# Optimization experiments

Hardware: AMD Instinct MI355X
Metric: run time of the kernel (lower is better)

Reference implementation:

```python
import jax, jax.numpy as jnp
import numpy as np

B, N, D, H, M, CD = 2, 2048, 1024, 16, 77, 768
DH = D // H          # head dim 64
FF = 4 * D           # GEGLU hidden 4096
NBITS = 8
EPS = 1e-5


def fake_quant_w(w, n_bits=NBITS):
    """Per-tensor uniform affine INT8 fake-quant (UniformAffineQuantizerINT8) with STE."""
    levels = 2 ** n_bits - 1
    mn = jnp.min(w)
    mx = jnp.max(w)
    delta = (mx - mn) / levels
    zp = jnp.round(-mn / delta)
    wq = jnp.clip(jnp.round(w / delta) + zp, 0, levels)
    wdq = (wq - zp) * delta
    return w + jax.lax.stop_gradient(wdq - w)


def layernorm(x, g, b):
    mu = jnp.mean(x, axis=-1, keepdims=True)
    var = jnp.mean((x - mu) ** 2, axis=-1, keepdims=True)
    return (x - mu) * jax.lax.rsqrt(var + EPS) * g + b


def linear(x, w, b=None):
    y = x @ fake_quant_w(w).T
    return y if b is None else y + b


def cross_attn(x, ctx, qw, kw, vw, ow, ob):
    Bq, Nq, _ = x.shape
    Nk = ctx.shape[1]
    q = linear(x, qw).reshape(Bq, Nq, H, DH)     # b n h d
    k = linear(ctx, kw).reshape(Bq, Nk, H, DH)
    v = linear(ctx, vw).reshape(Bq, Nk, H, DH)
    scale = DH ** -0.5
    sim = jnp.einsum('bihd,bjhd->bhij', q, k) * scale   # [B,H,Nq,Nk]
    attn = jax.nn.softmax(sim, axis=-1)
    out = jnp.einsum('bhij,bjhd->bihd', attn, v).reshape(Bq, Nq, D)
    return linear(out, ow, ob)


def geglu_ff(x, w1, b1, w2, b2):
    h = linear(x, w1, b1)                # [B,N,2*FF]
    hidden, gate = jnp.split(h, 2, axis=-1)
    return linear(hidden * jax.nn.gelu(gate), w2, b2)


def setup_inputs() -> dict:
    key = jax.random.key(0)
    ks = jax.random.split(key, 24)
    W = lambda k, o, i: (jax.random.normal(k, (o, i), jnp.float32) * 0.02)
    return {
        'x': jax.random.normal(ks[0], (B, N, D), jnp.float32),
        'context': jax.random.normal(ks[1], (B, M, CD), jnp.float32),
        'ln1_g': 1.0 + 0.1 * jax.random.normal(ks[2], (D,), jnp.float32),
        'ln1_b': 0.1 * jax.random.normal(ks[3], (D,), jnp.float32),
        'ln2_g': 1.0 + 0.1 * jax.random.normal(ks[4], (D,), jnp.float32),
        'ln2_b': 0.1 * jax.random.normal(ks[5], (D,), jnp.float32),
        'ln3_g': 1.0 + 0.1 * jax.random.normal(ks[6], (D,), jnp.float32),
        'ln3_b': 0.1 * jax.random.normal(ks[7], (D,), jnp.float32),
        'q1_w': W(ks[8], D, D), 'k1_w': W(ks[9], D, D), 'v1_w': W(ks[10], D, D),
        'o1_w': W(ks[11], D, D), 'o1_b': jnp.zeros((D,), jnp.float32),
        'q2_w': W(ks[12], D, D), 'k2_w': W(ks[13], D, CD), 'v2_w': W(ks[14], D, CD),
        'o2_w': W(ks[15], D, D), 'o2_b': jnp.zeros((D,), jnp.float32),
        'ff1_w': W(ks[16], 2 * FF, D), 'ff1_b': jnp.zeros((2 * FF,), jnp.float32),
        'ff2_w': W(ks[17], D, FF), 'ff2_b': jnp.zeros((D,), jnp.float32),
    }


def reference(x, context, ln1_g, ln1_b, ln2_g, ln2_b, ln3_g, ln3_b,
              q1_w, k1_w, v1_w, o1_w, o1_b,
              q2_w, k2_w, v2_w, o2_w, o2_b,
              ff1_w, ff1_b, ff2_w, ff2_b):
    x = cross_attn(layernorm(x, ln1_g, ln1_b), layernorm(x, ln1_g, ln1_b),
                   q1_w, k1_w, v1_w, o1_w, o1_b) + x
    x = cross_attn(layernorm(x, ln2_g, ln2_b), context,
                   q2_w, k2_w, v2_w, o2_w, o2_b) + x
    x = geglu_ff(layernorm(x, ln3_g, ln3_b), ff1_w, ff1_b, ff2_w, ff2_b) + x
    return x
```

## Files before the change

kernel.cpp:

```cpp
#include <hip/hip_runtime.h>
#include <cstdint>
#include <cstddef>

typedef unsigned short ushort_t;
typedef short s16x8 __attribute__((ext_vector_type(8)));
typedef float f32x4 __attribute__((ext_vector_type(4)));
typedef unsigned u32x4 __attribute__((ext_vector_type(4)));

#define MFMA(A,B,C) __builtin_amdgcn_mfma_f32_16x16x32_bf16((A),(B),(C),0,0,0)

__device__ __forceinline__ float b2f(ushort_t h){ return __uint_as_float(((unsigned)h)<<16); }
__device__ __forceinline__ ushort_t f2b(float f){
  unsigned u = __float_as_uint(f);
  u += 0x7FFFu + ((u >> 16) & 1u);
  return (ushort_t)(u >> 16);
}
__device__ __forceinline__ unsigned f2o(float f){
  unsigned u = __float_as_uint(f);
  return (u & 0x80000000u) ? ~u : (u | 0x80000000u);
}
__device__ __forceinline__ float o2f(unsigned u){
  unsigned b = (u & 0x80000000u) ? (u & 0x7FFFFFFFu) : ~u;
  return __uint_as_float(b);
}

struct QT { const float* w[10]; ushort_t* o[10]; int n[10]; };

__global__ void init_k(unsigned* slots){
  int t = threadIdx.x;
  if (t < 20) slots[t] = (t & 1) ? 0u : 0xFFFFFFFFu;
}

__global__ __launch_bounds__(256) void minmax_k(QT qt, unsigned* slots){
  int t = blockIdx.y;
  const float4* w = (const float4*)qt.w[t];
  int n4 = qt.n[t] >> 2;
  float mn = 3.4e38f, mx = -3.4e38f;
  for (int i = blockIdx.x*256 + threadIdx.x; i < n4; i += gridDim.x*256){
    float4 v = w[i];
    mn = fminf(mn, fminf(fminf(v.x, v.y), fminf(v.z, v.w)));
    mx = fmaxf(mx, fmaxf(fmaxf(v.x, v.y), fmaxf(v.z, v.w)));
  }
  #pragma unroll
  for (int o = 1; o < 64; o <<= 1){
    mn = fminf(mn, __shfl_xor(mn, o));
    mx = fmaxf(mx, __shfl_xor(mx, o));
  }
  __shared__ float smn[4], smx[4];
  int wv = threadIdx.x >> 6;
  if ((threadIdx.x & 63) == 0){ smn[wv] = mn; smx[wv] = mx; }
  __syncthreads();
  if (threadIdx.x == 0){
    mn = fminf(fminf(smn[0], smn[1]), fminf(smn[2], smn[3]));
    mx = fmaxf(fmaxf(smx[0], smx[1]), fmaxf(smx[2], smx[3]));
    atomicMin(&slots[2*t], f2o(mn));
    atomicMax(&slots[2*t+1], f2o(mx));
  }
}

__global__ __launch_bounds__(256) void dequant_k(QT qt, const unsigned* __restrict__ slots){
  int t = blockIdx.y;
  float mn = o2f(slots[2*t]), mx = o2f(slots[2*t+1]);
  float delta = (mx - mn) * (1.f/255.f);
  float zp = rintf(-mn / delta);
  const float4* w = (const float4*)qt.w[t];
  ushort4* o = (ushort4*)qt.o[t];
  int n4 = qt.n[t] >> 2;
  for (int i = blockIdx.x*256 + threadIdx.x; i < n4; i += gridDim.x*256){
    float4 v = w[i];
    ushort4 r;
    float q;
    q = fminf(fmaxf(rintf(v.x/delta) + zp, 0.f), 255.f); r.x = f2b((q - zp)*delta);
    q = fminf(fmaxf(rintf(v.y/delta) + zp, 0.f), 255.f); r.y = f2b((q - zp)*delta);
    q = fminf(fmaxf(rintf(v.z/delta) + zp, 0.f), 255.f); r.z = f2b((q - zp)*delta);
    q = fminf(fmaxf(rintf(v.w/delta) + zp, 0.f), 255.f); r.w = f2b((q - zp)*delta);
    o[i] = r;
  }
}

__global__ __launch_bounds__(256) void f2b_k(const float* __restrict__ in, ushort_t* __restrict__ out, int n4){
  for (int i = blockIdx.x*256 + threadIdx.x; i < n4; i += gridDim.x*256){
    float4 v = ((const float4*)in)[i];
    ushort4 r; r.x = f2b(v.x); r.y = f2b(v.y); r.z = f2b(v.z); r.w = f2b(v.w);
    ((ushort4*)out)[i] = r;
  }
}

__global__ __launch_bounds__(256) void ln_k(const float* __restrict__ x, const float* __restrict__ g,
                                            const float* __restrict__ b, ushort_t* __restrict__ out){
  int row = blockIdx.x, tid = threadIdx.x;
  float4 v = ((const float4*)(x + (size_t)row*1024))[tid];
  float s  = v.x + v.y + v.z + v.w;
  float s2 = v.x*v.x + v.y*v.y + v.z*v.z + v.w*v.w;
  #pragma unroll
  for (int o = 1; o < 64; o <<= 1){ s += __shfl_xor(s, o); s2 += __shfl_xor(s2, o); }
  __shared__ float rs[4], rs2[4];
  int wv = tid >> 6;
  if ((tid & 63) == 0){ rs[wv] = s; rs2[wv] = s2; }
  __syncthreads();
  s = rs[0]+rs[1]+rs[2]+rs[3]; s2 = rs2[0]+rs2[1]+rs2[2]+rs2[3];
  float mu = s * (1.f/1024.f);
  float var = s2 * (1.f/1024.f) - mu*mu;
  float rstd = rsqrtf(var + 1e-5f);
  float4 gv = ((const float4*)g)[tid], bv = ((const float4*)b)[tid];
  ushort4 r;
  r.x = f2b((v.x - mu)*rstd*gv.x + bv.x);
  r.y = f2b((v.y - mu)*rstd*gv.y + bv.y);
  r.z = f2b((v.z - mu)*rstd*gv.z + bv.z);
  r.w = f2b((v.w - mu)*rstd*gv.w + bv.w);
  ((ushort4*)(out + (size_t)row*1024))[tid] = r;
}

__global__ __launch_bounds__(512) void gemm_k(
    const ushort_t* __restrict__ A, const ushort_t* __restrict__ W,
    const float* __restrict__ bias, const float* __restrict__ resid,
    float* __restrict__ outF, ushort_t* __restrict__ outB,
    int M, int N, int K, int lda, int ldw)
{
  __shared__ ushort_t As[3][256*32];
  __shared__ ushort_t Bs[3][128*32];
  const int tid = threadIdx.x;
  const int lane = tid & 63, wv = tid >> 6;
  const int g = lane >> 4, qi = lane & 15;

  const int gx = gridDim.x, gy = gridDim.y;
  const int lid = blockIdx.x + blockIdx.y * gx;
  int m0, n0;
  if (((gx & 3) | (gy & 1)) == 0){
    const int w = gx >> 2, h = gy >> 1;
    const int xcd = lid & 7, o = lid >> 3;
    const int cx = xcd & 3, cy = xcd >> 2;
    n0 = (cx * w + (o % w)) * 128;
    m0 = (cy * h + (o / w)) * 256;
  } else {
    n0 = blockIdx.x * 128;
    m0 = blockIdx.y * 256;
  }

  const int koff = blockIdx.z * K;
  if (gridDim.z > 1) outF += (size_t)blockIdx.z * M * N;

  const int wr = (wv >> 1) * 64, wc = (wv & 1) * 64;
  f32x4 acc[4][4] = {};

  const int ra0 = tid >> 2,        sa0 = (tid & 3) ^ ((ra0 >> 1) & 3);
  const int ra1 = (512+tid) >> 2,  sa1 = ((512+tid) & 3) ^ ((ra1 >> 1) & 3);
  const int aA0 = (m0 + ra0 < M) ? m0 + ra0 : M - 1;
  const int aA1 = (m0 + ra1 < M) ? m0 + ra1 : M - 1;
  const size_t dA0 = (size_t)tid*8, dA1 = (size_t)(512+tid)*8, dB0 = (size_t)tid*8;

  #define GSTAGE(bi_, kt_) do {                                                    \
    __builtin_amdgcn_global_load_lds(                                              \
      (const __attribute__((address_space(1))) void*)(A + (size_t)aA0*lda + koff + (kt_) + sa0*8), \
      (__attribute__((address_space(3))) void*)(&As[bi_][dA0]), 16, 0, 0);         \
    __builtin_amdgcn_global_load_lds(                                              \
      (const __attribute__((address_space(1))) void*)(A + (size_t)aA1*lda + koff + (kt_) + sa1*8), \
      (__attribute__((address_space(3))) void*)(&As[bi_][dA1]), 16, 0, 0);         \
    __builtin_amdgcn_global_load_lds(                                              \
      (const __attribute__((address_space(1))) void*)(W + (size_t)(n0 + ra0)*ldw + koff + (kt_) + sa0*8), \
      (__attribute__((address_space(3))) void*)(&Bs[bi_][dB0]), 16, 0, 0);         \
  } while(0)

  const int nt = K >> 5;
  GSTAGE(0, 0);
  if (nt > 1) GSTAGE(1, 32);
  if (nt > 1) asm volatile("s_waitcnt vmcnt(3)" ::: "memory");
  else        asm volatile("s_waitcnt vmcnt(0)" ::: "memory");
  __builtin_amdgcn_s_barrier();
  __builtin_amdgcn_sched_barrier(0);

  int bi = 0;
  for (int t = 0; t < nt; ++t){
    int b2 = bi + 2; if (b2 >= 3) b2 -= 3;
    if (t + 2 < nt) GSTAGE(b2, (t + 2) << 5);
    s16x8 af[4], bfr[4];
    #pragma unroll
    for (int mi = 0; mi < 4; ++mi){
      int row = wr + mi*16 + qi;
      int sl = g ^ ((row >> 1) & 3);
      af[mi] = *(const s16x8*)(&As[bi][row*32 + sl*8]);
    }
    #pragma unroll
    for (int ni = 0; ni < 4; ++ni){
      int row = wc + ni*16 + qi;
      int sl = g ^ ((row >> 1) & 3);
      bfr[ni] = *(const s16x8*)(&Bs[bi][row*32 + sl*8]);
    }
    __builtin_amdgcn_s_setprio(1);
    #pragma unroll
    for (int mi = 0; mi < 4; ++mi)
      #pragma unroll
      for (int ni = 0; ni < 4; ++ni)
        acc[mi][ni] = MFMA(af[mi], bfr[ni], acc[mi][ni]);
    __builtin_amdgcn_s_setprio(0);
    if (t + 1 < nt){
      if (t + 2 < nt) asm volatile("s_waitcnt vmcnt(3)" ::: "memory");
      else            asm volatile("s_waitcnt vmcnt(0)" ::: "memory");
      __builtin_amdgcn_s_barrier();
      __builtin_amdgcn_sched_barrier(0);
    }
    bi += 1; if (bi >= 3) bi -= 3;
  }
  #undef GSTAGE

  #pragma unroll
  for (int mi = 0; mi < 4; ++mi){
    #pragma unroll
    for (int r = 0; r < 4; ++r){
      int row = m0 + wr + mi*16 + g*4 + r;
      if (row >= M) continue;
      #pragma unroll
      for (int ni = 0; ni < 4; ++ni){
        int col = n0 + wc + ni*16 + qi;
        float v = acc[mi][ni][r];
        if (bias)  v += bias[col];
        if (resid) v += resid[(size_t)row*N + col];
        if (outF)  outF[(size_t)row*N + col] = v;
        else       outB[(size_t)row*N + col] = f2b(v);
      }
    }
  }
}

__global__ __launch_bounds__(256) void reduce_k(const float* __restrict__ p0, const float* __restrict__ p1,
                                                const float* __restrict__ bias, const float* __restrict__ resid,
                                                float* __restrict__ outF, ushort_t* __restrict__ outB, int n4){
  for (int i = blockIdx.x*256 + threadIdx.x; i < n4; i += gridDim.x*256){
    float4 a = ((const float4*)p0)[i];
    float4 b = ((const float4*)p1)[i];
    float4 v;
    v.x = a.x + b.x; v.y = a.y + b.y; v.z = a.z + b.z; v.w = a.w + b.w;
    if (bias){
      float4 bb = ((const float4*)bias)[i & 255];
      v.x += bb.x; v.y += bb.y; v.z += bb.z; v.w += bb.w;
    }
    if (resid){
      float4 r = ((const float4*)resid)[i];
      v.x += r.x; v.y += r.y; v.z += r.z; v.w += r.w;
    }
    if (outF) ((float4*)outF)[i] = v;
    else {
      ushort4 o; o.x = f2b(v.x); o.y = f2b(v.y); o.z = f2b(v.z); o.w = f2b(v.w);
      ((ushort4*)outB)[i] = o;
    }
  }
}

__global__ __launch_bounds__(256) void vtrans_k(const ushort_t* __restrict__ src, ushort_t* __restrict__ dst,
                                                int rows, int stride, int col_off, int nk_pad){
  __shared__ ushort_t ldst[64*130];
  int n0 = blockIdx.x * 128;
  int b = blockIdx.y >> 4, h = blockIdx.y & 15;
  const ushort_t* s = src + (size_t)b*rows*stride + col_off + h*64;
  for (int idx = threadIdx.x; idx < 128*64; idx += 256){
    int n = idx >> 6, d = idx & 63;
    int ng = n0 + n;
    ushort_t v = (ng < rows) ? s[(size_t)ng*stride + d] : (ushort_t)0;
    ldst[d*130 + n] = v;
  }
  __syncthreads();
  ushort_t* o = dst + (size_t)(b*16 + h)*64*nk_pad;
  for (int idx = threadIdx.x; idx < 64*128; idx += 256){
    int d = idx >> 7, n = idx & 127;
    if (n0 + n < nk_pad) o[(size_t)d*nk_pad + n0 + n] = ldst[d*130 + n];
  }
}

__global__ __launch_bounds__(256) void attn_k(
    const ushort_t* __restrict__ Q, const ushort_t* __restrict__ Kp, const ushort_t* __restrict__ Vt,
    ushort_t* __restrict__ O, int nq, int nk, int qstride, int kvstride, int nk_pad)
{
  __shared__ ushort_t Ks[2][32*64];
  __shared__ ushort_t Vs[2][64*32];
  const int tid = threadIdx.x, lane = tid & 63, wv = tid >> 6;
  const int g = lane >> 4, qi = lane & 15;
  const int b = blockIdx.y >> 4, h = blockIdx.y & 15;
  const int q0 = blockIdx.x*64 + wv*16;

  const ushort_t* Qr = Q + (size_t)(b*nq + q0 + qi)*qstride + h*64;
  s16x8 qf0 = *(const s16x8*)(Qr + g*8);
  s16x8 qf1 = *(const s16x8*)(Qr + 32 + g*8);
  const ushort_t* Kb = Kp + (size_t)b*nk*kvstride + h*64;
  const ushort_t* Vb = Vt + (size_t)(b*16 + h)*64*nk_pad;

  const int krow = wv*8 + (lane >> 3);
  const int kgsl = (lane & 7) ^ (krow & 7);
  const int vrow = wv*16 + (lane >> 2);
  const int vgsl = (lane & 3) ^ ((vrow >> 1) & 3);

  #define STAGE(buf, kb_) do {                                                   \
    int kr_ = (kb_) + krow; if (kr_ >= nk) kr_ = nk - 1;                         \
    __builtin_amdgcn_global_load_lds(                                            \
      (const __attribute__((address_space(1))) void*)(Kb + (size_t)kr_*kvstride + kgsl*8), \
      (__attribute__((address_space(3))) void*)(&Ks[buf][(size_t)wv*512]), 16, 0, 0); \
    __builtin_amdgcn_global_load_lds(                                            \
      (const __attribute__((address_space(1))) void*)(Vb + (size_t)vrow*nk_pad + (kb_) + vgsl*8), \
      (__attribute__((address_space(3))) void*)(&Vs[buf][(size_t)wv*512]), 16, 0, 0); \
  } while(0)

  const int nkp = (nk + 31) & ~31;
  f32x4 ot[4] = {};
  float m_run = -1e30f, l_run = 0.f;
  const float SC = 0.18033688011f;

  const int ks0 = (g     ^ (qi & 7)) * 8;
  const int ks1 = ((4+g) ^ (qi & 7)) * 8;
  const int vs0 = (g ^ ((qi >> 1) & 3)) * 8;

  STAGE(0, 0);
  asm volatile("s_waitcnt vmcnt(0)" ::: "memory");
  __syncthreads();
  int cur = 0;
  for (int kb = 0; kb < nkp; kb += 32){
    if (kb + 32 < nkp) STAGE(cur^1, kb + 32);
    s16x8 ka0 = *(const s16x8*)(&Ks[cur][(qi)*64      + ks0]);
    s16x8 ka1 = *(const s16x8*)(&Ks[cur][(qi)*64      + ks1]);
    s16x8 kb0 = *(const s16x8*)(&Ks[cur][(16+qi)*64   + ks0]);
    s16x8 kb1 = *(const s16x8*)(&Ks[cur][(16+qi)*64   + ks1]);
    s16x8 vf0 = *(const s16x8*)(&Vs[cur][(qi)*32      + vs0]);
    s16x8 vf1 = *(const s16x8*)(&Vs[cur][(16+qi)*32   + vs0]);
    s16x8 vf2 = *(const s16x8*)(&Vs[cur][(32+qi)*32   + vs0]);
    s16x8 vf3 = *(const s16x8*)(&Vs[cur][(48+qi)*32   + vs0]);

    f32x4 st0 = {}, st1 = {};
    st0 = MFMA(ka0, qf0, st0);
    st0 = MFMA(ka1, qf1, st0);
    st1 = MFMA(kb0, qf0, st1);
    st1 = MFMA(kb1, qf1, st1);
    float s[8];
    #pragma unroll
    for (int r = 0; r < 4; ++r){ s[r] = st0[r]*SC; s[4+r] = st1[r]*SC; }
    if (kb + 32 > nk){
      #pragma unroll
      for (int r = 0; r < 4; ++r){
        if (kb + 4*g + r >= nk)      s[r]   = -1e30f;
        if (kb + 16 + 4*g + r >= nk) s[4+r] = -1e30f;
      }
    }
    float bm = fmaxf(fmaxf(fmaxf(s[0], s[1]), fmaxf(s[2], s[3])),
                     fmaxf(fmaxf(s[4], s[5]), fmaxf(s[6], s[7])));
    bm = fmaxf(bm, __shfl_xor(bm, 16));
    bm = fmaxf(bm, __shfl_xor(bm, 32));
    if (!__all(bm <= m_run)){
      float m_new = fmaxf(m_run, bm);
      float fac = exp2f(m_run - m_new);
      l_run *= fac;
      #pragma unroll
      for (int dd = 0; dd < 4; ++dd)
        #pragma unroll
        for (int r = 0; r < 4; ++r) ot[dd][r] *= fac;
      m_run = m_new;
    }
    float p[8], rsum = 0.f;
    #pragma unroll
    for (int i = 0; i < 8; ++i){ p[i] = exp2f(s[i] - m_run); rsum += p[i]; }
    rsum += __shfl_xor(rsum, 16);
    rsum += __shfl_xor(rsum, 32);
    l_run += rsum;
    unsigned pk[4];
    #pragma unroll
    for (int r = 0; r < 4; ++r)
      pk[r] = (unsigned)f2b(p[r]) | ((unsigned)f2b(p[4+r]) << 16);
    int srcbase = ((2*g) & 3) * 16 + qi;
    unsigned sh0[4], sh1[4];
    #pragma unroll
    for (int r = 0; r < 4; ++r){
      sh0[r] = (unsigned)__shfl((int)pk[r], srcbase);
      sh1[r] = (unsigned)__shfl((int)pk[r], srcbase + 16);
    }
    unsigned sel = (g >> 1) ? 0x07060302u : 0x05040100u;
    u32x4 pw;
    pw[0] = __builtin_amdgcn_perm(sh0[1], sh0[0], sel);
    pw[1] = __builtin_amdgcn_perm(sh0[3], sh0[2], sel);
    pw[2] = __builtin_amdgcn_perm(sh1[1], sh1[0], sel);
    pw[3] = __builtin_amdgcn_perm(sh1[3], sh1[2], sel);
    s16x8 pf = __builtin_bit_cast(s16x8, pw);
    ot[0] = MFMA(vf0, pf, ot[0]);
    ot[1] = MFMA(vf1, pf, ot[1]);
    ot[2] = MFMA(vf2, pf, ot[2]);
    ot[3] = MFMA(vf3, pf, ot[3]);

    asm volatile("s_waitcnt vmcnt(0)" ::: "memory");
    __syncthreads();
    cur ^= 1;
  }
  #undef STAGE
  float inv = 1.f / l_run;
  ushort_t* Or = O + (size_t)(b*nq + q0 + qi)*1024 + h*64;
  #pragma unroll
  for (int dd = 0; dd < 4; ++dd)
    #pragma unroll
    for (int r = 0; r < 4; ++r)
      Or[dd*16 + 4*g + r] = f2b(ot[dd][r] * inv);
}

__global__ __launch_bounds__(256) void geglu_k(const ushort_t* __restrict__ h, ushort_t* __restrict__ out){
  int idx = blockIdx.x*256 + threadIdx.x;
  int r = idx >> 9, c = idx & 511;
  s16x8 hv = *(const s16x8*)(h + (size_t)r*8192 + c*8);
  s16x8 gv = *(const s16x8*)(h + (size_t)r*8192 + 4096 + c*8);
  s16x8 o;
  #pragma unroll
  for (int i = 0; i < 8; ++i){
    float gg = b2f((ushort_t)gv[i]);
    float t  = 0.7978845608f*(gg + 0.044715f*gg*gg*gg);
    float e  = __expf(2.f*t);
    float th = 1.f - 2.f/(e + 1.f);
    float ge = 0.5f*gg*(1.f + th);
    o[i] = (short)f2b(b2f((ushort_t)hv[i]) * ge);
  }
  *(s16x8*)(out + (size_t)r*4096 + c*8) = o;
}

extern "C" void kernel_launch(void* const* d_in, const int* in_sizes, int n_in,
                              void* d_out, int out_size, void* d_ws, size_t ws_size,
                              hipStream_t stream)
{
  const float* x    = (const float*)d_in[0];
  const float* ctx  = (const float*)d_in[1];
  const float* ln1g = (const float*)d_in[2];
  const float* ln1b = (const float*)d_in[3];
  const float* ln2g = (const float*)d_in[4];
  const float* ln2b = (const float*)d_in[5];
  const float* ln3g = (const float*)d_in[6];
  const float* ln3b = (const float*)d_in[7];
  const float* q1w  = (const float*)d_in[8];
  const float* k1w  = (const float*)d_in[9];
  const float* v1w  = (const float*)d_in[10];
  const float* o1w  = (const float*)d_in[11];
  const float* o1b  = (const float*)d_in[12];
  const float* q2w  = (const float*)d_in[13];
  const float* k2w  = (const float*)d_in[14];
  const float* v2w  = (const float*)d_in[15];
  const float* o2w  = (const float*)d_in[16];
  const float* o2b  = (const float*)d_in[17];
  const float* ff1w = (const float*)d_in[18];
  const float* ff1b = (const float*)d_in[19];
  const float* ff2w = (const float*)d_in[20];
  const float* ff2b = (const float*)d_in[21];

  char* base = (char*)d_ws;
  size_t off = 0;
  auto alloc = [&](size_t bytes) -> char* {
    char* p = base + off;
    off += (bytes + 255) & ~(size_t)255;
    return p;
  };
  unsigned*  slots = (unsigned*)alloc(80);
  ushort_t*  ctxb  = (ushort_t*)alloc((size_t)154*768*2);
  ushort_t*  wqkv1 = (ushort_t*)alloc((size_t)3072*1024*2);
  ushort_t*  o1d   = (ushort_t*)alloc((size_t)1024*1024*2);
  ushort_t*  q2d   = (ushort_t*)alloc((size_t)1024*1024*2);
  ushort_t*  wkv2  = (ushort_t*)alloc((size_t)2048*768*2);
  ushort_t*  o2d   = (ushort_t*)alloc((size_t)1024*1024*2);
  ushort_t*  f1d   = (ushort_t*)alloc((size_t)8192*1024*2);
  ushort_t*  f2d   = (ushort_t*)alloc((size_t)1024*4096*2);
  ushort_t*  lnb   = (ushort_t*)alloc((size_t)4096*1024*2);
  ushort_t*  qkvb  = (ushort_t*)alloc((size_t)4096*3072*2);
  ushort_t*  q2b   = (ushort_t*)alloc((size_t)4096*1024*2);
  ushort_t*  atb   = (ushort_t*)alloc((size_t)4096*1024*2);
  ushort_t*  kvb   = (ushort_t*)alloc((size_t)154*2048*2);
  ushort_t*  vt1   = (ushort_t*)alloc((size_t)2*16*64*2048*2);
  ushort_t*  vt2   = (ushort_t*)alloc((size_t)2*16*64*96*2);
  float*     x1    = (float*)alloc((size_t)4096*1024*4);
  float*     x2    = (float*)alloc((size_t)4096*1024*4);
  ushort_t*  hb    = (ushort_t*)alloc((size_t)4096*8192*2);
  ushort_t*  actb  = qkvb;
  float*     part  = (float*)hb;
  float*     part1 = part + (size_t)4096*1024;

  QT qt;
  qt.w[0]=q1w;  qt.o[0]=wqkv1;               qt.n[0]=1024*1024;
  qt.w[1]=k1w;  qt.o[1]=wqkv1+1024*1024;     qt.n[1]=1024*1024;
  qt.w[2]=v1w;  qt.o[2]=wqkv1+2*1024*1024;   qt.n[2]=1024*1024;
  qt.w[3]=o1w;  qt.o[3]=o1d;                 qt.n[3]=1024*1024;
  qt.w[4]=q2w;  qt.o[4]=q2d;                 qt.n[4]=1024*1024;
  qt.w[5]=k2w;  qt.o[5]=wkv2;                qt.n[5]=1024*768;
  qt.w[6]=v2w;  qt.o[6]=wkv2+1024*768;       qt.n[6]=1024*768;
  qt.w[7]=o2w;  qt.o[7]=o2d;                 qt.n[7]=1024*1024;
  qt.w[8]=ff1w; qt.o[8]=f1d;                 qt.n[8]=8192*1024;
  qt.w[9]=ff2w; qt.o[9]=f2d;                 qt.n[9]=1024*4096;

  init_k<<<1, 64, 0, stream>>>(slots);
  minmax_k<<<dim3(64,10), 256, 0, stream>>>(qt, slots);
  dequant_k<<<dim3(64,10), 256, 0, stream>>>(qt, slots);
  f2b_k<<<64, 256, 0, stream>>>(ctx, ctxb, 154*768/4);

  ln_k<<<4096, 256, 0, stream>>>(x, ln1g, ln1b, lnb);
  gemm_k<<<dim3(24, 16), 512, 0, stream>>>(lnb, wqkv1, nullptr, nullptr,
                                           nullptr, qkvb, 4096, 3072, 1024, 1024, 1024);
  vtrans_k<<<dim3(16, 32), 256, 0, stream>>>(qkvb, vt1, 2048, 3072, 2048, 2048);
  attn_k<<<dim3(32, 32), 256, 0, stream>>>(qkvb, qkvb+1024, vt1, atb,
                                           2048, 2048, 3072, 3072, 2048);
  gemm_k<<<dim3(8, 16, 2), 512, 0, stream>>>(atb, o1d, nullptr, nullptr,
                                             part, nullptr, 4096, 1024, 512, 1024, 1024);
  reduce_k<<<2048, 256, 0, stream>>>(part, part1, o1b, x, x1, nullptr, 4096*1024/4);

  ln_k<<<4096, 256, 0, stream>>>(x1, ln2g, ln2b, lnb);
  gemm_k<<<dim3(8, 16, 2), 512, 0, stream>>>(lnb, q2d, nullptr, nullptr,
                                             part, nullptr, 4096, 1024, 512, 1024, 1024);
  reduce_k<<<2048, 256, 0, stream>>>(part, part1, nullptr, nullptr, nullptr, q2b, 4096*1024/4);
  gemm_k<<<dim3(16, 1), 512, 0, stream>>>(ctxb, wkv2, nullptr, nullptr,
                                          nullptr, kvb, 154, 2048, 768, 768, 768);
  vtrans_k<<<dim3(1, 32), 256, 0, stream>>>(kvb, vt2, 77, 2048, 1024, 96);
  attn_k<<<dim3(32, 32), 256, 0, stream>>>(q2b, kvb, vt2, atb,
                                           2048, 77, 1024, 2048, 96);
  gemm_k<<<dim3(8, 16, 2), 512, 0, stream>>>(atb, o2d, nullptr, nullptr,
                                             part, nullptr, 4096, 1024, 512, 1024, 1024);
  reduce_k<<<2048, 256, 0, stream>>>(part, part1, o2b, x1, x2, nullptr, 4096*1024/4);

  ln_k<<<4096, 256, 0, stream>>>(x2, ln3g, ln3b, lnb);
  gemm_k<<<dim3(64, 16), 512, 0, stream>>>(lnb, f1d, ff1b, nullptr,
                                           nullptr, hb, 4096, 8192, 1024, 1024, 1024);
  geglu_k<<<8192, 256, 0, stream>>>(hb, actb);
  gemm_k<<<dim3(8, 16, 2), 512, 0, stream>>>(actb, f2d, nullptr, nullptr,
                                             part, nullptr, 4096, 1024, 2048, 4096, 4096);
  reduce_k<<<2048, 256, 0, stream>>>(part, part1, ff2b, x2,
                                     (float*)d_out, nullptr, 4096*1024/4);
}
```

Measured before the change: 633.2 us.

## Fold softmax scale into Q weights and enlarge attention blocks to 8 waves

The softmax scale (including log2e) is folded into the dequantized Q projection weights, which removes the per-score multiply inside attention. Attention blocks grow from 4 to 8 waves covering 128 queries, so each K/V tile staged in shared memory serves twice as many queries, and the staging work is split so four waves load K and four load V. exp2f is replaced by the hardware exp2 builtin. Folding the scale before bf16 rounding of the weights changes rounding slightly, and the larger blocks halve the grid, which may reduce occupancy.

```diff
diff --git a/kernel.cpp b/kernel.cpp
--- a/kernel.cpp
+++ b/kernel.cpp
@@ -24,7 +24,7 @@
   return __uint_as_float(b);
 }
 
-struct QT { const float* w[10]; ushort_t* o[10]; int n[10]; };
+struct QT { const float* w[10]; ushort_t* o[10]; int n[10]; float os[10]; };
 
 __global__ void init_k(unsigned* slots){
   int t = threadIdx.x;
@@ -63,6 +63,7 @@
   float mn = o2f(slots[2*t]), mx = o2f(slots[2*t+1]);
   float delta = (mx - mn) * (1.f/255.f);
   float zp = rintf(-mn / delta);
+  float osc = qt.os[t];
   const float4* w = (const float4*)qt.w[t];
   ushort4* o = (ushort4*)qt.o[t];
   int n4 = qt.n[t] >> 2;
@@ -70,10 +71,10 @@
     float4 v = w[i];
     ushort4 r;
     float q;
-    q = fminf(fmaxf(rintf(v.x/delta) + zp, 0.f), 255.f); r.x = f2b((q - zp)*delta);
-    q = fminf(fmaxf(rintf(v.y/delta) + zp, 0.f), 255.f); r.y = f2b((q - zp)*delta);
-    q = fminf(fmaxf(rintf(v.z/delta) + zp, 0.f), 255.f); r.z = f2b((q - zp)*delta);
-    q = fminf(fmaxf(rintf(v.w/delta) + zp, 0.f), 255.f); r.w = f2b((q - zp)*delta);
+    q = fminf(fmaxf(rintf(v.x/delta) + zp, 0.f), 255.f); r.x = f2b((q - zp)*delta*osc);
+    q = fminf(fmaxf(rintf(v.y/delta) + zp, 0.f), 255.f); r.y = f2b((q - zp)*delta*osc);
+    q = fminf(fmaxf(rintf(v.z/delta) + zp, 0.f), 255.f); r.z = f2b((q - zp)*delta*osc);
+    q = fminf(fmaxf(rintf(v.w/delta) + zp, 0.f), 255.f); r.w = f2b((q - zp)*delta*osc);
     o[i] = r;
   }
 }
@@ -266,7 +267,7 @@
   }
 }
 
-__global__ __launch_bounds__(256) void attn_k(
+__global__ __launch_bounds__(512) void attn_k(
     const ushort_t* __restrict__ Q, const ushort_t* __restrict__ Kp, const ushort_t* __restrict__ Vt,
     ushort_t* __restrict__ O, int nq, int nk, int qstride, int kvstride, int nk_pad)
 {
@@ -275,7 +276,7 @@
   const int tid = threadIdx.x, lane = tid & 63, wv = tid >> 6;
   const int g = lane >> 4, qi = lane & 15;
   const int b = blockIdx.y >> 4, h = blockIdx.y & 15;
-  const int q0 = blockIdx.x*64 + wv*16;
+  const int q0 = blockIdx.x*128 + wv*16;
 
   const ushort_t* Qr = Q + (size_t)(b*nq + q0 + qi)*qstride + h*64;
   s16x8 qf0 = *(const s16x8*)(Qr + g*8);
@@ -283,25 +284,27 @@
   const ushort_t* Kb = Kp + (size_t)b*nk*kvstride + h*64;
   const ushort_t* Vb = Vt + (size_t)(b*16 + h)*64*nk_pad;
 
-  const int krow = wv*8 + (lane >> 3);
+  const int krow = (wv & 3)*8 + (lane >> 3);
   const int kgsl = (lane & 7) ^ (krow & 7);
-  const int vrow = wv*16 + (lane >> 2);
+  const int vrow = (wv & 3)*16 + (lane >> 2);
   const int vgsl = (lane & 3) ^ ((vrow >> 1) & 3);
 
   #define STAGE(buf, kb_) do {                                                   \
-    int kr_ = (kb_) + krow; if (kr_ >= nk) kr_ = nk - 1;                         \
-    __builtin_amdgcn_global_load_lds(                                            \
-      (const __attribute__((address_space(1))) void*)(Kb + (size_t)kr_*kvstride + kgsl*8), \
-      (__attribute__((address_space(3))) void*)(&Ks[buf][(size_t)wv*512]), 16, 0, 0); \
-    __builtin_amdgcn_global_load_lds(                                            \
-      (const __attribute__((address_space(1))) void*)(Vb + (size_t)vrow*nk_pad + (kb_) + vgsl*8), \
-      (__attribute__((address_space(3))) void*)(&Vs[buf][(size_t)wv*512]), 16, 0, 0); \
+    if (wv < 4){                                                                 \
+      int kr_ = (kb_) + krow; if (kr_ >= nk) kr_ = nk - 1;                       \
+      __builtin_amdgcn_global_load_lds(                                          \
+        (const __attribute__((address_space(1))) void*)(Kb + (size_t)kr_*kvstride + kgsl*8), \
+        (__attribute__((address_space(3))) void*)(&Ks[buf][(size_t)(wv&3)*512]), 16, 0, 0); \
+    } else {                                                                     \
+      __builtin_amdgcn_global_load_lds(                                          \
+        (const __attribute__((address_space(1))) void*)(Vb + (size_t)vrow*nk_pad + (kb_) + vgsl*8), \
+        (__attribute__((address_space(3))) void*)(&Vs[buf][(size_t)(wv&3)*512]), 16, 0, 0); \
+    }                                                                            \
   } while(0)
 
   const int nkp = (nk + 31) & ~31;
   f32x4 ot[4] = {};
   float m_run = -1e30f, l_run = 0.f;
-  const float SC = 0.18033688011f;
 
   const int ks0 = (g     ^ (qi & 7)) * 8;
   const int ks1 = ((4+g) ^ (qi & 7)) * 8;
@@ -329,7 +332,7 @@
     st1 = MFMA(kb1, qf1, st1);
     float s[8];
     #pragma unroll
-    for (int r = 0; r < 4; ++r){ s[r] = st0[r]*SC; s[4+r] = st1[r]*SC; }
+    for (int r = 0; r < 4; ++r){ s[r] = st0[r]; s[4+r] = st1[r]; }
     if (kb + 32 > nk){
       #pragma unroll
       for (int r = 0; r < 4; ++r){
@@ -343,7 +346,7 @@
     bm = fmaxf(bm, __shfl_xor(bm, 32));
     if (!__all(bm <= m_run)){
       float m_new = fmaxf(m_run, bm);
-      float fac = exp2f(m_run - m_new);
+      float fac = __builtin_amdgcn_exp2f(m_run - m_new);
       l_run *= fac;
       #pragma unroll
       for (int dd = 0; dd < 4; ++dd)
@@ -353,7 +356,7 @@
     }
     float p[8], rsum = 0.f;
     #pragma unroll
-    for (int i = 0; i < 8; ++i){ p[i] = exp2f(s[i] - m_run); rsum += p[i]; }
+    for (int i = 0; i < 8; ++i){ p[i] = __builtin_amdgcn_exp2f(s[i] - m_run); rsum += p[i]; }
     rsum += __shfl_xor(rsum, 16);
     rsum += __shfl_xor(rsum, 32);
     l_run += rsum;
@@ -469,17 +472,18 @@
   float*     part  = (float*)hb;
   float*     part1 = part + (size_t)4096*1024;
 
+  const float SC = 0.18033688011f;
   QT qt;
-  qt.w[0]=q1w;  qt.o[0]=wqkv1;               qt.n[0]=1024*1024;
-  qt.w[1]=k1w;  qt.o[1]=wqkv1+1024*1024;     qt.n[1]=1024*1024;
-  qt.w[2]=v1w;  qt.o[2]=wqkv1+2*1024*1024;   qt.n[2]=1024*1024;
-  qt.w[3]=o1w;  qt.o[3]=o1d;                 qt.n[3]=1024*1024;
-  qt.w[4]=q2w;  qt.o[4]=q2d;                 qt.n[4]=1024*1024;
-  qt.w[5]=k2w;  qt.o[5]=wkv2;                qt.n[5]=1024*768;
-  qt.w[6]=v2w;  qt.o[6]=wkv2+1024*768;       qt.n[6]=1024*768;
-  qt.w[7]=o2w;  qt.o[7]=o2d;                 qt.n[7]=1024*1024;
-  qt.w[8]=ff1w; qt.o[8]=f1d;                 qt.n[8]=8192*1024;
-  qt.w[9]=ff2w; qt.o[9]=f2d;                 qt.n[9]=1024*4096;
+  qt.w[0]=q1w;  qt.o[0]=wqkv1;               qt.n[0]=1024*1024; qt.os[0]=SC;
+  qt.w[1]=k1w;  qt.o[1]=wqkv1+1024*1024;     qt.n[1]=1024*1024; qt.os[1]=1.f;
+  qt.w[2]=v1w;  qt.o[2]=wqkv1+2*1024*1024;   qt.n[2]=1024*1024; qt.os[2]=1.f;
+  qt.w[3]=o1w;  qt.o[3]=o1d;                 qt.n[3]=1024*1024; qt.os[3]=1.f;
+  qt.w[4]=q2w;  qt.o[4]=q2d;                 qt.n[4]=1024*1024; qt.os[4]=SC;
+  qt.w[5]=k2w;  qt.o[5]=wkv2;                qt.n[5]=1024*768;  qt.os[5]=1.f;
+  qt.w[6]=v2w;  qt.o[6]=wkv2+1024*768;       qt.n[6]=1024*768;  qt.os[6]=1.f;
+  qt.w[7]=o2w;  qt.o[7]=o2d;                 qt.n[7]=1024*1024; qt.os[7]=1.f;
+  qt.w[8]=ff1w; qt.o[8]=f1d;                 qt.n[8]=8192*1024; qt.os[8]=1.f;
+  qt.w[9]=ff2w; qt.o[9]=f2d;                 qt.n[9]=1024*4096; qt.os[9]=1.f;
 
   init_k<<<1, 64, 0, stream>>>(slots);
   minmax_k<<<dim3(64,10), 256, 0, stream>>>(qt, slots);
@@ -490,7 +494,7 @@
   gemm_k<<<dim3(24, 16), 512, 0, stream>>>(lnb, wqkv1, nullptr, nullptr,
                                            nullptr, qkvb, 4096, 3072, 1024, 1024, 1024);
   vtrans_k<<<dim3(16, 32), 256, 0, stream>>>(qkvb, vt1, 2048, 3072, 2048, 2048);
-  attn_k<<<dim3(32, 32), 256, 0, stream>>>(qkvb, qkvb+1024, vt1, atb,
+  attn_k<<<dim3(16, 32), 512, 0, stream>>>(qkvb, qkvb+1024, vt1, atb,
                                            2048, 2048, 3072, 3072, 2048);
   gemm_k<<<dim3(8, 16, 2), 512, 0, stream>>>(atb, o1d, nullptr, nullptr,
                                              part, nullptr, 4096, 1024, 512, 1024, 1024);
@@ -503,7 +507,7 @@
   gemm_k<<<dim3(16, 1), 512, 0, stream>>>(ctxb, wkv2, nullptr, nullptr,
                                           nullptr, kvb, 154, 2048, 768, 768, 768);
   vtrans_k<<<dim3(1, 32), 256, 0, stream>>>(kvb, vt2, 77, 2048, 1024, 96);
-  attn_k<<<dim3(32, 32), 256, 0, stream>>>(q2b, kvb, vt2, atb,
+  attn_k<<<dim3(16, 32), 512, 0, stream>>>(q2b, kvb, vt2, atb,
                                            2048, 77, 1024, 2048, 96);
   gemm_k<<<dim3(8, 16, 2), 512, 0, stream>>>(atb, o2d, nullptr, nullptr,
                                              part, nullptr, 4096, 1024, 512, 1024, 1024);
```

Measured after the change: 601.2 us. -5.1%, faster.
